# Kernel tuning notes

Hardware: AMD Instinct MI355X
Metric: run time of the kernel (lower is better)

The kernel has to match this reference:

```python
import jax, jax.numpy as jnp
import numpy as np

DIM = 2048
HIDDEN = 2048
HEADS = 4
HD = HIDDEN // HEADS  # head_dim = 512
EPS = 1e-6
BATCH = 4
SEQ = 2048


def setup_inputs() -> dict:
    key = jax.random.key(0)
    k0, k1, k2, k3 = jax.random.split(key, 4)
    s = 0.02  # typical init scale; keeps exp() input gate well-behaved
    x = jax.random.normal(k0, (BATCH, SEQ, DIM), dtype=jnp.float32)
    W_in = (jax.random.normal(k1, (HIDDEN, DIM), dtype=jnp.float32) * s)
    W_gate = (jax.random.normal(k2, (4 * HIDDEN, HIDDEN), dtype=jnp.float32) * s)
    b_gate = jnp.zeros((4 * HIDDEN,), dtype=jnp.float32)
    rms_w = jnp.ones((HD,), dtype=jnp.float32)
    W_out = (jax.random.normal(k3, (DIM, HIDDEN), dtype=jnp.float32) * s)
    return {"x": x, "W_in": W_in, "W_gate": W_gate, "b_gate": b_gate,
            "rms_w": rms_w, "W_out": W_out}


def reference(x, W_in, W_gate, b_gate, rms_w, W_out):
    B, L, _ = x.shape
    # in_proj then gate_proj (the rearrange round-trip in torch is an identity
    # on the flat hidden dim, so gates come straight from x @ W_in.T)
    xp = x @ W_in.T                                    # (B, L, HIDDEN)
    gates = xp @ W_gate.T + b_gate                     # (B, L, 4*HIDDEN)
    # rearrange 'b l (h d) -> b h l d' with h=HEADS, d=4*HD
    gates = gates.reshape(B, L, HEADS, 4 * HD).transpose(0, 2, 1, 3)
    i_g, f_g, o_g, c_t = jnp.split(gates, 4, axis=-1)  # each (B, H, L, HD)
    i_g = jnp.exp(i_g)            # exponential input gate
    f_g = jax.nn.sigmoid(f_g)
    o_g = jax.nn.sigmoid(o_g)
    c_t = jnp.tanh(c_t)

    # time-major for the recurrent scan: (L, B, H, HD)
    tm = lambda a: jnp.moveaxis(a, 2, 0)

    def step(c, g):
        i, f, o, cd = g
        c = f * c + i * cd                                         # cell update
        c_norm = c * jax.lax.rsqrt(jnp.mean(c * c, axis=-1, keepdims=True) + EPS) * rms_w
        h = o * jnp.tanh(c_norm)
        return c, h

    c0 = jnp.zeros((B, HEADS, HD), dtype=x.dtype)
    _, hs = jax.lax.scan(step, c0, (tm(i_g), tm(f_g), tm(o_g), tm(c_t)))
    # (L, B, H, HD) -> (B, L, H*HD)
    h_out = jnp.moveaxis(hs, 0, 1).reshape(B, L, HIDDEN)
    return h_out @ W_out.T                             # (B, L, DIM)
```

## Files before the change

### kernel.cpp

```cpp
#include <hip/hip_runtime.h>
#include <hip/hip_bf16.h>
#include <stdint.h>

#define DIMN    2048
#define HIDDEN  2048
#define NHEADS  4
#define HDIM    512
#define BATCH   4
#define SEQ     2048
#define NTOK    (BATCH*SEQ)
#define G4      (4*HIDDEN)
#define EPSV    1e-6f

typedef short short8 __attribute__((ext_vector_type(8)));
typedef float floatx4 __attribute__((ext_vector_type(4)));

union BV8 { uint4 u; __hip_bfloat16 h[8]; unsigned short s[8]; };

__device__ __forceinline__ float fast_sigmoid(float x) {
    return 1.0f / (1.0f + __expf(-x));
}
__device__ __forceinline__ float fast_tanh(float x) {
    return 1.0f - 2.0f / (__expf(2.0f * x) + 1.0f);
}
__device__ __forceinline__ float b2f(unsigned short u) {
    union { unsigned int ui; float f; } v; v.ui = ((unsigned int)u) << 16; return v.f;
}

__device__ __forceinline__ void gld_lds16(const void* gp, void* lp) {
    __builtin_amdgcn_global_load_lds(
        (const __attribute__((address_space(1))) void*)gp,
        (__attribute__((address_space(3))) void*)lp, 16, 0, 0);
}

__global__ __launch_bounds__(256) void cast_f32_bf16(
    const float* __restrict__ in, __hip_bfloat16* __restrict__ out, int n8)
{
    int i = blockIdx.x * 256 + threadIdx.x;
    if (i >= n8) return;
    const float4* p = (const float4*)(in + (size_t)i * 8);
    float4 a = p[0], b = p[1];
    BV8 v;
    v.h[0] = __float2bfloat16(a.x); v.h[1] = __float2bfloat16(a.y);
    v.h[2] = __float2bfloat16(a.z); v.h[3] = __float2bfloat16(a.w);
    v.h[4] = __float2bfloat16(b.x); v.h[5] = __float2bfloat16(b.y);
    v.h[6] = __float2bfloat16(b.z); v.h[7] = __float2bfloat16(b.w);
    *(uint4*)(out + (size_t)i * 8) = v.u;
}

template <int EPILOGUE, int ASRC>
__global__ __launch_bounds__(256) void gemm_bt(
    const __hip_bfloat16* __restrict__ A,
    const __hip_bfloat16* __restrict__ Bt,
    void* __restrict__ Cout,
    const float* __restrict__ bias,
    int M, int N, int K, int lda)
{
    const int bm = blockIdx.y, bn = blockIdx.x;
    const int tid = threadIdx.x;
    const int wave = tid >> 6, lane = tid & 63;
    const int wm = wave >> 1, wn = wave & 1;
    const int quad = lane >> 4, lr = lane & 15;

    __shared__ __align__(16) short sA[128 * 64];
    __shared__ __align__(16) short sB[128 * 64];

    floatx4 acc[4][4];
#pragma unroll
    for (int i = 0; i < 4; ++i)
#pragma unroll
        for (int j = 0; j < 4; ++j) acc[i][j] = (floatx4)0.0f;

    const short* Ag = (const short*)A + (size_t)(bm * 128) * lda;
    const short* Bg = (const short*)Bt + (size_t)(bn * 128) * K;

    const int r8  = lane >> 3;
    const int gcs = ((lane & 7) ^ r8) * 8;
    const int rl7 = lr & 7;

    for (int kb = 0; kb < K; kb += 64) {
        size_t acol;
        if (ASRC == 0) acol = (size_t)(kb + gcs);
        else           acol = (size_t)(((kb >> 9) * 2048) + (kb & 511) + gcs);
#pragma unroll
        for (int it = 0; it < 4; ++it) {
            const int rowb = wave * 32 + it * 8;
            const int grow = rowb + r8;
            gld_lds16(Ag + (size_t)grow * lda + acol,       &sA[rowb * 64]);
            gld_lds16(Bg + (size_t)grow * K + kb + gcs,     &sB[rowb * 64]);
        }
        __syncthreads();
#pragma unroll
        for (int kc = 0; kc < 2; ++kc) {
            const int q = kc * 4 + quad;
            const int co = ((q ^ rl7) << 3);
            short8 af[4], bfr[4];
#pragma unroll
            for (int mt = 0; mt < 4; ++mt)
                af[mt] = *(const short8*)&sA[(wm * 64 + mt * 16 + lr) * 64 + co];
#pragma unroll
            for (int nt = 0; nt < 4; ++nt)
                bfr[nt] = *(const short8*)&sB[(wn * 64 + nt * 16 + lr) * 64 + co];
#pragma unroll
            for (int mt = 0; mt < 4; ++mt)
#pragma unroll
                for (int nt = 0; nt < 4; ++nt)
                    acc[mt][nt] = __builtin_amdgcn_mfma_f32_16x16x32_bf16(
                        af[mt], bfr[nt], acc[mt][nt], 0, 0, 0);
        }
        __syncthreads();
    }

    const int colbase = bn * 128 + wn * 64;
    const int rowbase = bm * 128 + wm * 64;

    if (EPILOGUE == 0) {
        __hip_bfloat16* O = (__hip_bfloat16*)Cout;
#pragma unroll
        for (int mt = 0; mt < 4; ++mt)
#pragma unroll
            for (int nt = 0; nt < 4; ++nt)
#pragma unroll
                for (int r = 0; r < 4; ++r) {
                    int row = rowbase + mt * 16 + quad * 4 + r;
                    int col = colbase + nt * 16 + lr;
                    O[(size_t)row * N + col] = __float2bfloat16(acc[mt][nt][r]);
                }
    } else if (EPILOGUE == 1) {
        __hip_bfloat16* O = (__hip_bfloat16*)Cout;
#pragma unroll
        for (int nt = 0; nt < 4; ++nt) {
            int col = colbase + nt * 16 + lr;
            int g = (col >> 9) & 3;
            float bv = bias[col];
#pragma unroll
            for (int mt = 0; mt < 4; ++mt)
#pragma unroll
                for (int r = 0; r < 4; ++r) {
                    int row = rowbase + mt * 16 + quad * 4 + r;
                    float v = acc[mt][nt][r] + bv;
                    if (g == 0)       v = __expf(v);
                    else if (g == 3)  v = fast_tanh(v);
                    else              v = fast_sigmoid(v);
                    O[(size_t)row * N + col] = __float2bfloat16(v);
                }
        }
    } else {
        float* O = (float*)Cout;
#pragma unroll
        for (int mt = 0; mt < 4; ++mt)
#pragma unroll
            for (int nt = 0; nt < 4; ++nt)
#pragma unroll
                for (int r = 0; r < 4; ++r) {
                    int row = rowbase + mt * 16 + quad * 4 + r;
                    int col = colbase + nt * 16 + lr;
                    O[(size_t)row * N + col] = acc[mt][nt][r];
                }
    }
}

struct G16 { unsigned short i[16], f[16], c[16]; };

__device__ __forceinline__ void load_g16(const unsigned short* __restrict__ g,
                                         int t0, G16& o)
{
#pragma unroll
    for (int j = 0; j < 16; ++j) {
        const unsigned short* gp = g + (size_t)(t0 + j) * G4;
        o.i[j] = gp[0]; o.f[j] = gp[512]; o.c[j] = gp[1536];
    }
}
__device__ __forceinline__ float comp_g16(const G16& gg, float c,
                                          __hip_bfloat16* __restrict__ cb, int t0)
{
#pragma unroll
    for (int j = 0; j < 16; ++j) {
        float iv = b2f(gg.i[j]);
        float fv = b2f(gg.f[j]);
        float cd = b2f(gg.c[j]);
        c = fmaf(fv, c, iv * cd);
        cb[(size_t)(t0 + j) * HIDDEN] = __float2bfloat16(c);
    }
    return c;
}

__global__ __launch_bounds__(64) void scan_kernel(
    const __hip_bfloat16* __restrict__ gates, __hip_bfloat16* __restrict__ cbuf)
{
    int blk = blockIdx.x;
    int bh = blk >> 3, dc = blk & 7;
    int b = bh >> 2, h = bh & 3;
    int d = dc * 64 + threadIdx.x;
    const unsigned short* g = (const unsigned short*)gates
        + (size_t)b * SEQ * G4 + h * 2048 + d;
    __hip_bfloat16* cb = cbuf + (size_t)b * SEQ * HIDDEN + h * 512 + d;

    G16 A, B;
    load_g16(g, 0, A);
    float c = 0.0f;
    for (int t0 = 0; t0 < SEQ; t0 += 32) {
        load_g16(g, t0 + 16, B);
        c = comp_g16(A, c, cb, t0);
        if (t0 + 32 < SEQ) load_g16(g, t0 + 32, A);
        c = comp_g16(B, c, cb, t0 + 16);
    }
}

__global__ __launch_bounds__(64) void norm_kernel(
    const __hip_bfloat16* __restrict__ cbuf, __hip_bfloat16* __restrict__ gates,
    const float* __restrict__ rms_w)
{
    int blk = blockIdx.x;
    int h = blk & 3;
    int t = (blk >> 2) & (SEQ - 1);
    int b = blk >> 13;
    int lane = threadIdx.x;
    size_t tok = (size_t)(b * SEQ + t);

    BV8 cv; cv.u = *(const uint4*)(cbuf + tok * HIDDEN + h * 512 + lane * 8);
    float cf[8]; float s = 0.0f;
#pragma unroll
    for (int j = 0; j < 8; ++j) { cf[j] = b2f(cv.s[j]); s += cf[j] * cf[j]; }
#pragma unroll
    for (int off = 32; off > 0; off >>= 1) s += __shfl_xor(s, off, 64);
    float rs = rsqrtf(s * (1.0f / 512.0f) + EPSV);

    BV8 ov; ov.u = *(const uint4*)(gates + tok * G4 + h * 2048 + 1024 + lane * 8);
    float4 w0 = *(const float4*)&rms_w[lane * 8];
    float4 w1 = *(const float4*)&rms_w[lane * 8 + 4];
    float w[8] = { w0.x, w0.y, w0.z, w0.w, w1.x, w1.y, w1.z, w1.w };

    BV8 hv;
#pragma unroll
    for (int j = 0; j < 8; ++j) {
        float o = b2f(ov.s[j]);
        hv.h[j] = __float2bfloat16(o * fast_tanh(cf[j] * rs * w[j]));
    }
    *(uint4*)(gates + tok * G4 + h * 2048 + lane * 8) = hv.u;
}

extern "C" void kernel_launch(void* const* d_in, const int* in_sizes, int n_in,
                              void* d_out, int out_size, void* d_ws, size_t ws_size,
                              hipStream_t stream)
{
    const float* x      = (const float*)d_in[0];
    const float* W_in   = (const float*)d_in[1];
    const float* W_gate = (const float*)d_in[2];
    const float* b_gate = (const float*)d_in[3];
    const float* rms_w  = (const float*)d_in[4];
    const float* W_out  = (const float*)d_in[5];
    float* out = (float*)d_out;

    char* base = (char*)d_ws;
    __hip_bfloat16* wgb   = (__hip_bfloat16*)base;
    __hip_bfloat16* xpb   = (__hip_bfloat16*)(base + (((size_t)32) << 20));
    __hip_bfloat16* gates = (__hip_bfloat16*)(base + (((size_t)64) << 20));
    __hip_bfloat16* wib  = gates;
    __hip_bfloat16* xb   = (__hip_bfloat16*)(base + (((size_t)72) << 20));
    __hip_bfloat16* wob  = wgb;
    __hip_bfloat16* cbuf = xpb;

    cast_f32_bf16<<<(HIDDEN * DIMN) / 8 / 256, 256, 0, stream>>>(W_in, wib, (HIDDEN * DIMN) / 8);
    cast_f32_bf16<<<(NTOK * DIMN) / 8 / 256, 256, 0, stream>>>(x, xb, (NTOK * DIMN) / 8);
    cast_f32_bf16<<<(G4 * HIDDEN) / 8 / 256, 256, 0, stream>>>(W_gate, wgb, (G4 * HIDDEN) / 8);

    {
        dim3 grid(HIDDEN / 128, NTOK / 128);
        gemm_bt<0, 0><<<grid, 256, 0, stream>>>(xb, wib, xpb, nullptr,
                                                NTOK, HIDDEN, DIMN, DIMN);
    }
    {
        dim3 grid(G4 / 128, NTOK / 128);
        gemm_bt<1, 0><<<grid, 256, 0, stream>>>(xpb, wgb, gates, b_gate,
                                                NTOK, G4, HIDDEN, HIDDEN);
    }
    cast_f32_bf16<<<(DIMN * HIDDEN) / 8 / 256, 256, 0, stream>>>(W_out, wob, (DIMN * HIDDEN) / 8);

    scan_kernel<<<BATCH * NHEADS * 8, 64, 0, stream>>>(gates, cbuf);

    norm_kernel<<<BATCH * SEQ * NHEADS, 64, 0, stream>>>(cbuf, gates, rms_w);

    {
        dim3 grid(DIMN / 128, NTOK / 128);
        gemm_bt<2, 1><<<grid, 256, 0, stream>>>(gates, wob, out, nullptr,
                                                NTOK, DIMN, HIDDEN, G4);
    }
}
```

Before: 757.8 us.

## Replace sequential cell scan with two-pass chunked parallel scan

The single sequential scan over 2048 timesteps (128 blocks of 64 threads) is split into 16 chunks of 128 steps. The first pass computes, per chunk, the local final cell state and the running product of forget gates. The second pass combines earlier chunks' summaries to get the incoming state, then re-runs its chunk and writes the cell states. This exposes far more parallelism to hide the latency of the recurrence, at the cost of reading the gate tensor twice and adding a small fp32 workspace for the chunk summaries.

```diff
diff --git a/kernel.cpp b/kernel.cpp
--- a/kernel.cpp
+++ b/kernel.cpp
@@ -11,6 +11,8 @@
 #define NTOK    (BATCH*SEQ)
 #define G4      (4*HIDDEN)
 #define EPSV    1e-6f
+#define CHUNK   128
+#define NCHUNK  (SEQ/CHUNK)
 
 typedef short short8 __attribute__((ext_vector_type(8)));
 typedef float floatx4 __attribute__((ext_vector_type(4)));
@@ -171,8 +173,19 @@
         o.i[j] = gp[0]; o.f[j] = gp[512]; o.c[j] = gp[1536];
     }
 }
-__device__ __forceinline__ float comp_g16(const G16& gg, float c,
-                                          __hip_bfloat16* __restrict__ cb, int t0)
+__device__ __forceinline__ void comp_sum16(const G16& gg, float& c, float& P)
+{
+#pragma unroll
+    for (int j = 0; j < 16; ++j) {
+        float iv = b2f(gg.i[j]);
+        float fv = b2f(gg.f[j]);
+        float cd = b2f(gg.c[j]);
+        c = fmaf(fv, c, iv * cd);
+        P *= fv;
+    }
+}
+__device__ __forceinline__ float comp_store16(const G16& gg, float c,
+                                              __hip_bfloat16* __restrict__ cb, int t0)
 {
 #pragma unroll
     for (int j = 0; j < 16; ++j) {
@@ -185,25 +198,63 @@
     return c;
 }
 
-__global__ __launch_bounds__(64) void scan_kernel(
-    const __hip_bfloat16* __restrict__ gates, __hip_bfloat16* __restrict__ cbuf)
+__global__ __launch_bounds__(256) void scan_pass1(
+    const __hip_bfloat16* __restrict__ gates,
+    float* __restrict__ cLast, float* __restrict__ PLast)
 {
     int blk = blockIdx.x;
-    int bh = blk >> 3, dc = blk & 7;
+    int dh = blk & 1;
+    int j  = (blk >> 1) & 15;
+    int bh = blk >> 5;
     int b = bh >> 2, h = bh & 3;
-    int d = dc * 64 + threadIdx.x;
+    int d = dh * 256 + threadIdx.x;
+    int bhd = bh * 512 + d;
+
     const unsigned short* g = (const unsigned short*)gates
-        + (size_t)b * SEQ * G4 + h * 2048 + d;
-    __hip_bfloat16* cb = cbuf + (size_t)b * SEQ * HIDDEN + h * 512 + d;
-
+        + (size_t)(b * SEQ + j * CHUNK) * G4 + h * 2048 + d;
+
+    float c = 0.0f, P = 1.0f;
     G16 A, B;
     load_g16(g, 0, A);
+    for (int t0 = 0; t0 < CHUNK; t0 += 32) {
+        load_g16(g, t0 + 16, B);
+        comp_sum16(A, c, P);
+        if (t0 + 32 < CHUNK) load_g16(g, t0 + 32, A);
+        comp_sum16(B, c, P);
+    }
+    cLast[j * 8192 + bhd] = c;
+    PLast[j * 8192 + bhd] = P;
+}
+
+__global__ __launch_bounds__(256) void scan_pass2(
+    const __hip_bfloat16* __restrict__ gates,
+    const float* __restrict__ cLast, const float* __restrict__ PLast,
+    __hip_bfloat16* __restrict__ cbuf)
+{
+    int blk = blockIdx.x;
+    int dh = blk & 1;
+    int j  = (blk >> 1) & 15;
+    int bh = blk >> 5;
+    int b = bh >> 2, h = bh & 3;
+    int d = dh * 256 + threadIdx.x;
+    int bhd = bh * 512 + d;
+
     float c = 0.0f;
-    for (int t0 = 0; t0 < SEQ; t0 += 32) {
+    for (int k = 0; k < j; ++k)
+        c = fmaf(PLast[k * 8192 + bhd], c, cLast[k * 8192 + bhd]);
+
+    const unsigned short* g = (const unsigned short*)gates
+        + (size_t)(b * SEQ + j * CHUNK) * G4 + h * 2048 + d;
+    __hip_bfloat16* cb = cbuf
+        + (size_t)(b * SEQ + j * CHUNK) * HIDDEN + h * 512 + d;
+
+    G16 A, B;
+    load_g16(g, 0, A);
+    for (int t0 = 0; t0 < CHUNK; t0 += 32) {
         load_g16(g, t0 + 16, B);
-        c = comp_g16(A, c, cb, t0);
-        if (t0 + 32 < SEQ) load_g16(g, t0 + 32, A);
-        c = comp_g16(B, c, cb, t0 + 16);
+        c = comp_store16(A, c, cb, t0);
+        if (t0 + 32 < CHUNK) load_g16(g, t0 + 32, A);
+        c = comp_store16(B, c, cb, t0 + 16);
     }
 }
 
@@ -259,6 +310,8 @@
     __hip_bfloat16* wib  = gates;
     __hip_bfloat16* xb   = (__hip_bfloat16*)(base + (((size_t)72) << 20));
     __hip_bfloat16* wob  = wgb;
+    float* cLast = (float*)(base + (((size_t)8) << 20));
+    float* PLast = (float*)(base + (((size_t)8) << 20) + (512 << 10));
     __hip_bfloat16* cbuf = xpb;
 
     cast_f32_bf16<<<(HIDDEN * DIMN) / 8 / 256, 256, 0, stream>>>(W_in, wib, (HIDDEN * DIMN) / 8);
@@ -277,7 +330,8 @@
     }
     cast_f32_bf16<<<(DIMN * HIDDEN) / 8 / 256, 256, 0, stream>>>(W_out, wob, (DIMN * HIDDEN) / 8);
 
-    scan_kernel<<<BATCH * NHEADS * 8, 64, 0, stream>>>(gates, cbuf);
+    scan_pass1<<<BATCH * NHEADS * NCHUNK * 2, 256, 0, stream>>>(gates, cLast, PLast);
+    scan_pass2<<<BATCH * NHEADS * NCHUNK * 2, 256, 0, stream>>>(gates, cLast, PLast, cbuf);
 
     norm_kernel<<<BATCH * SEQ * NHEADS, 64, 0, stream>>>(cbuf, gates, rms_w);
 
```

After: 734.2 us. 3.1% less time.
